# Optimization experiments

Measured on AMD Instinct MI355X. Metric: run time of the kernel, lower is better.

Reference implementation:

```python
import jax, jax.numpy as jnp
import numpy as np

N_NODES = 50000
N_EDGES = 800000
N_GRAPHS = 64
IN_DIM = 128
HID4 = 256  # hidden_dim * 4
OUT_DIM = 256
EPS = 1e-5


def setup_inputs() -> dict:
    key = jax.random.key(0)
    ks = jax.random.split(key, 11)
    x = jax.random.normal(ks[0], (N_NODES, IN_DIM), jnp.float32)
    w = jax.random.uniform(ks[1], (N_EDGES,), jnp.float32)
    src = jax.random.randint(ks[2], (N_EDGES,), 0, N_NODES, dtype=jnp.int32)
    dst = jax.random.randint(ks[3], (N_EDGES,), 0, N_NODES, dtype=jnp.int32)
    graph_ids = jnp.sort(jax.random.randint(ks[4], (N_NODES,), 0, N_GRAPHS, dtype=jnp.int32))
    W1 = jax.random.normal(ks[5], (IN_DIM, HID4), jnp.float32) * 0.05
    Wfc = jax.random.normal(ks[6], (IN_DIM, HID4), jnp.float32) * 0.05
    gamma = jnp.ones((HID4,), jnp.float32)
    beta = jnp.zeros((HID4,), jnp.float32)
    W2 = jax.random.normal(ks[7], (2 * HID4, HID4), jnp.float32) * 0.05
    W3 = jax.random.normal(ks[8], (HID4, OUT_DIM), jnp.float32) * 0.05
    return {"x": x, "w": w, "W1": W1, "Wfc": Wfc, "gamma": gamma, "beta": beta,
            "W2": W2, "W3": W3, "src": src, "dst": dst, "graph_ids": graph_ids}


def _agg(h, src, dst, w, n):
    # edge-weighted SpMM: sum_{e: dst(e)=v} w_e * h[src(e)]
    return jax.ops.segment_sum(h[src] * w[:, None], dst, num_segments=n)


def _graph_conv(h, W, src, dst, w, out_norm, in_norm, n):
    # DGL GraphConv, norm='both', no bias, with edge_weight.
    h = h * out_norm  # D_out^{-1/2} on source side
    din, dout = W.shape
    if din > dout:  # DGL applies W first when it shrinks the width
        h = _agg(h @ W, src, dst, w, n)
    else:
        h = _agg(h, src, dst, w, n) @ W
    return h * in_norm  # D_in^{-1/2} on destination side


def _layer_norm(h, gamma, beta):
    mu = jnp.mean(h, axis=-1, keepdims=True)
    var = jnp.var(h, axis=-1, keepdims=True)
    return (h - mu) * jax.lax.rsqrt(var + EPS) * gamma + beta


def reference(x, w, W1, Wfc, gamma, beta, W2, W3, src, dst, graph_ids):
    n = x.shape[0]
    ones_e = jnp.ones(src.shape[0], jnp.float32)
    out_deg = jnp.maximum(jax.ops.segment_sum(ones_e, src, num_segments=n), 1.0)
    in_deg = jnp.maximum(jax.ops.segment_sum(ones_e, dst, num_segments=n), 1.0)
    out_norm = (out_deg ** -0.5)[:, None]
    in_norm = (in_deg ** -0.5)[:, None]

    x1 = jax.nn.relu(_graph_conv(x, W1, src, dst, w, out_norm, in_norm, n))
    f1 = jax.nn.relu(_layer_norm(x @ Wfc, gamma, beta))
    x1f1 = jnp.concatenate((x1, f1), axis=1)  # [N, 512]
    x2 = jax.nn.relu(_graph_conv(x1f1, W2, src, dst, w, out_norm, in_norm, n))
    x3 = jax.nn.relu(_graph_conv(x2, W3, src, dst, w, out_norm, in_norm, n))
    # dgl.sum_nodes: per-graph segment-sum readout
    readout = jax.ops.segment_sum(x3, graph_ids, num_segments=N_GRAPHS)
    return readout
```

## Files before the change

### kernel.cpp

```cpp
#include <hip/hip_runtime.h>

#define NN 50000
#define NE 800000
#define NG 64
#define EPSF 1e-5f

typedef __bf16 bf16x8 __attribute__((ext_vector_type(8)));
typedef float f32x4 __attribute__((ext_vector_type(4)));

#define AS1 __attribute__((address_space(1)))
#define AS3 __attribute__((address_space(3)))

__device__ __forceinline__ void gl_lds16(const unsigned short* g, unsigned short* l) {
#if __has_builtin(__builtin_amdgcn_global_load_lds)
  __builtin_amdgcn_global_load_lds((const AS1 void*)g, (AS3 void*)l, 16, 0, 0);
#else
  *(uint4*)l = *(const uint4*)g;
#endif
}

__device__ __forceinline__ unsigned short f2bf(float f) {
  unsigned u = __builtin_bit_cast(unsigned, f);
  u += 0x7fff + ((u >> 16) & 1);
  return (unsigned short)(u >> 16);
}
__device__ __forceinline__ float bf_lo(unsigned u) {
  return __builtin_bit_cast(float, u << 16);
}
__device__ __forceinline__ float bf_hi(unsigned u) {
  return __builtin_bit_cast(float, u & 0xffff0000u);
}

#define NB_H 64
#define EC   12500
#define HWORDS 12500
#define XB   1563
#define XTOT 1600000
#define WTB  256
__global__ __launch_bounds__(1024) void prep_kernel(
    const int* __restrict__ src, const int* __restrict__ dst,
    unsigned char* __restrict__ hout, unsigned char* __restrict__ hin,
    int* __restrict__ rank,
    const float* __restrict__ x, unsigned short* __restrict__ xb,
    const float* __restrict__ W1, const float* __restrict__ Wfc,
    const float* __restrict__ W2, const float* __restrict__ W3,
    unsigned short* __restrict__ W1t, unsigned short* __restrict__ Wfct,
    unsigned short* __restrict__ W2t, unsigned short* __restrict__ W3t) {
  __shared__ unsigned hist[HWORDS];
  int b = blockIdx.x;
  int tid = threadIdx.x;
  if (b < NB_H) {
    int e0 = b * EC;
#pragma unroll
    for (int ph = 0; ph < 2; ph++) {
      const int* key = ph ? src : dst;
      unsigned char* gh = (ph ? hout : hin) + (size_t)b * NN;
      for (int i = tid; i < HWORDS; i += 1024) hist[i] = 0u;
      __syncthreads();
      for (int i = tid; i < EC; i += 1024) {
        int k = key[e0 + i];
        int sh = (k & 3) << 3;
        unsigned old = atomicAdd(&hist[k >> 2], 1u << sh);
        if (ph == 0) rank[e0 + i] = (int)((old >> sh) & 0xffu);
      }
      __syncthreads();
      unsigned* gw = (unsigned*)gh;
      for (int i = tid; i < HWORDS; i += 1024) gw[i] = hist[i];
      __syncthreads();
    }
  } else if (b < NB_H + XB) {
    int i = (b - NB_H) * 1024 + tid;
    if (i < XTOT) {
      float4 v = ((const float4*)x)[i];
      uint2 pk;
      pk.x = (unsigned)f2bf(v.x) | ((unsigned)f2bf(v.y) << 16);
      pk.y = (unsigned)f2bf(v.z) | ((unsigned)f2bf(v.w) << 16);
      ((uint2*)xb)[i] = pk;
    }
  } else {
    int i = (b - NB_H - XB) * 1024 + tid;
    const float* W; unsigned short* Wt; int K, local;
    if (i < 32768)       { W = W1;  Wt = W1t;  K = 128; local = i; }
    else if (i < 65536)  { W = Wfc; Wt = Wfct; K = 128; local = i - 32768; }
    else if (i < 196608) { W = W2;  Wt = W2t;  K = 512; local = i - 65536; }
    else                 { W = W3;  Wt = W3t;  K = 256; local = i - 196608; }
    int n = local / K, k = local - n * K;
    Wt[local] = f2bf(W[(size_t)k * 256 + n]);
  }
}

__global__ void norms_scan1(const unsigned char* __restrict__ hout,
                            unsigned char* __restrict__ hin,
                            int* __restrict__ din,
                            float* __restrict__ onorm, float* __restrict__ inorm,
                            int* __restrict__ bsum, int n) {
  int i = blockIdx.x * 256 + threadIdx.x;
  int d = 0;
  if (i < n) {
    int a = 0;
    for (int b = 0; b < NB_H; b++) a += hout[(size_t)b * NN + i];
    int run = 0;
    for (int b = 0; b < NB_H; b++) {
      int t = hin[(size_t)b * NN + i];
      hin[(size_t)b * NN + i] = (unsigned char)run;
      run += t;
    }
    d = run;
    din[i] = run;
    onorm[i] = rsqrtf((float)(a > 1 ? a : 1));
    inorm[i] = rsqrtf((float)(d > 1 ? d : 1));
  }
  int v = d;
#pragma unroll
  for (int off = 32; off > 0; off >>= 1) v += __shfl_down(v, off);
  __shared__ int ws[4];
  int wave = threadIdx.x >> 6, lane = threadIdx.x & 63;
  if (lane == 0) ws[wave] = v;
  __syncthreads();
  if (threadIdx.x == 0) bsum[blockIdx.x] = ws[0] + ws[1] + ws[2] + ws[3];
}

__global__ void scan3_kernel(const int* __restrict__ din, const int* __restrict__ bsum,
                             int* __restrict__ rp, int n, int nb) {
  int t = threadIdx.x;
  int lane = t & 63, wave = t >> 6;
  int bj = (t < nb) ? bsum[t] : 0;
  int pre = (t < (int)blockIdx.x) ? bj : 0;
  int p = pre, q = bj;
#pragma unroll
  for (int off = 32; off > 0; off >>= 1) {
    p += __shfl_down(p, off);
    q += __shfl_down(q, off);
  }
  __shared__ int red[8];
  __shared__ int baseS, totS;
  if (lane == 0) { red[wave] = p; red[4 + wave] = q; }
  __syncthreads();
  if (t == 0) {
    baseS = red[0] + red[1] + red[2] + red[3];
    totS  = red[4] + red[5] + red[6] + red[7];
  }
  __syncthreads();
  int i = blockIdx.x * 256 + t;
  int v = (i < n) ? din[i] : 0;
  __shared__ int tmp[256];
  tmp[t] = v;
  __syncthreads();
  for (int off = 1; off < 256; off <<= 1) {
    int x = (t >= off) ? tmp[t - off] : 0;
    __syncthreads();
    tmp[t] += x;
    __syncthreads();
  }
  if (i < n) rp[i] = tmp[t] - v + baseS;
  if (blockIdx.x == gridDim.x - 1 && t == 0) rp[n] = totS;
}

__global__ void fill_kernel(const int* __restrict__ src, const int* __restrict__ dst,
                            const float* __restrict__ w, const float* __restrict__ onorm,
                            const float* __restrict__ inorm,
                            const int* __restrict__ rp, const int* __restrict__ rank,
                            const unsigned char* __restrict__ binBase,
                            uint2* __restrict__ edge, int E) {
  int e = blockIdx.x * 256 + threadIdx.x;
  if (e < E) {
    int d = dst[e], s = src[e];
    int b = e / EC;
    int pos = rp[d] + (int)binBase[(size_t)b * NN + d] + rank[e];
    float wv = w[e] * onorm[s] * inorm[d];
    edge[pos] = make_uint2((unsigned)s, __builtin_bit_cast(unsigned, wv));
  }
}

template <int RELU, int NU>
__global__ __launch_bounds__(64) void spmm_bf16(
    const unsigned short* __restrict__ feat, int ldf,
    const int* __restrict__ rp, const uint2* __restrict__ edge,
    unsigned short* __restrict__ out, int ldo) {
  int v = blockIdx.x;
  int t = threadIdx.x;
  int beg = rp[v], end = rp[v + 1];
  float acc[2 * NU];
#pragma unroll
  for (int i = 0; i < 2 * NU; i++) acc[i] = 0.f;
  const unsigned short* base = feat + t * (2 * NU);
  int e = beg;
  for (; e + 8 <= end; e += 8) {
    int s[8]; float ww[8];
#pragma unroll
    for (int k = 0; k < 8; k++) {
      uint2 q = edge[e + k];
      s[k] = (int)q.x;
      ww[k] = __builtin_bit_cast(float, q.y);
    }
    unsigned u[8][NU];
#pragma unroll
    for (int k = 0; k < 8; k++) {
      const unsigned* pr = (const unsigned*)&base[(size_t)s[k] * ldf];
      if (NU == 2) { uint2 q = *(const uint2*)pr; u[k][0] = q.x; u[k][NU - 1] = q.y; }
      else u[k][0] = pr[0];
    }
#pragma unroll
    for (int k = 0; k < 8; k++)
#pragma unroll
      for (int j = 0; j < NU; j++) {
        acc[2 * j]     += ww[k] * bf_lo(u[k][j]);
        acc[2 * j + 1] += ww[k] * bf_hi(u[k][j]);
      }
  }
  for (; e < end; e++) {
    uint2 qe = edge[e];
    float w0 = __builtin_bit_cast(float, qe.y);
    const unsigned* pr = (const unsigned*)&base[(size_t)qe.x * ldf];
    unsigned u[NU];
    if (NU == 2) { uint2 q = *(const uint2*)pr; u[0] = q.x; u[NU - 1] = q.y; }
    else u[0] = pr[0];
#pragma unroll
    for (int j = 0; j < NU; j++) {
      acc[2 * j]     += w0 * bf_lo(u[j]);
      acc[2 * j + 1] += w0 * bf_hi(u[j]);
    }
  }
  unsigned o[NU];
#pragma unroll
  for (int j = 0; j < NU; j++) {
    float a = acc[2 * j], b = acc[2 * j + 1];
    if (RELU) { a = fmaxf(a, 0.f); b = fmaxf(b, 0.f); }
    o[j] = (unsigned)f2bf(a) | ((unsigned)f2bf(b) << 16);
  }
  unsigned* po = (unsigned*)&out[(size_t)v * ldo + t * (2 * NU)];
  if (NU == 2) *(uint2*)po = make_uint2(o[0], o[NU - 1]);
  else po[0] = o[0];
}

__device__ __forceinline__ void gemm256_body(
    const unsigned short* __restrict__ A, int lda,
    const unsigned short* __restrict__ Bt, int K,
    unsigned short* __restrict__ C, int ldc, int col_off, int M,
    int relu, unsigned short* As, unsigned short* Bs) {
  const int tid = threadIdx.x;
  const int lane = tid & 63;
  const int w = tid >> 6;
  const int q = lane >> 4;
  const int r16 = lane & 15;
  const int m0 = blockIdx.x * 128;

  f32x4 acc[8][4];
#pragma unroll
  for (int i = 0; i < 8; i++)
#pragma unroll
    for (int j = 0; j < 4; j++) acc[i][j] = (f32x4){0.f, 0.f, 0.f, 0.f};

  int ga0 = m0 + (2 * w) * 16 + r16;     if (ga0 >= M) ga0 = M - 1;
  int ga1 = m0 + (2 * w + 1) * 16 + r16; if (ga1 >= M) ga1 = M - 1;
  const unsigned short* pa0 = A + (size_t)ga0 * lda + q * 8;
  const unsigned short* pa1 = A + (size_t)ga1 * lda + q * 8;
  const unsigned short* pbt[4];
#pragma unroll
  for (int t = 0; t < 4; t++) {
    int gn = (4 * w + t) * 16 + r16;
    pbt[t] = Bt + (size_t)gn * K + q * 8;
  }

  for (int k0 = 0; k0 < K; k0 += 32) {
    __syncthreads();
    gl_lds16(pa0 + k0, &As[(2 * w) * 512 + lane * 8]);
    gl_lds16(pa1 + k0, &As[(2 * w + 1) * 512 + lane * 8]);
#pragma unroll
    for (int t = 0; t < 4; t++)
      gl_lds16(pbt[t] + k0, &Bs[(4 * w + t) * 512 + lane * 8]);
    __syncthreads();

    bf16x8 bfr[4];
#pragma unroll
    for (int j = 0; j < 4; j++)
      bfr[j] = *(const bf16x8*)&Bs[(4 * w + j) * 512 + lane * 8];
#pragma unroll
    for (int i = 0; i < 8; i++) {
      bf16x8 af = *(const bf16x8*)&As[i * 512 + lane * 8];
#pragma unroll
      for (int j = 0; j < 4; j++)
        acc[i][j] = __builtin_amdgcn_mfma_f32_16x16x32_bf16(af, bfr[j], acc[i][j], 0, 0, 0);
    }
  }

#pragma unroll
  for (int i = 0; i < 8; i++) {
    int rbase = m0 + i * 16 + q * 4;
#pragma unroll
    for (int r = 0; r < 4; r++) {
      int gm = rbase + r;
      if (gm >= M) continue;
#pragma unroll
      for (int j = 0; j < 4; j++) {
        float v = acc[i][j][r];
        if (relu) v = fmaxf(v, 0.f);
        int gn = col_off + (4 * w + j) * 16 + r16;
        C[(size_t)gm * ldc + gn] = f2bf(v);
      }
    }
  }
}

__global__ __launch_bounds__(256) void gemm12_kernel(
    const unsigned short* __restrict__ A0, const unsigned short* __restrict__ B0,
    const unsigned short* __restrict__ A1, const unsigned short* __restrict__ B1,
    unsigned short* __restrict__ C, int M) {
  __shared__ unsigned short As[8 * 512];
  __shared__ unsigned short Bs[16 * 512];
  int z = blockIdx.z;
  gemm256_body(z ? A1 : A0, 128, z ? B1 : B0, 128, C, 512, z * 256, M, z == 0, As, Bs);
}

__global__ __launch_bounds__(256) void gemm_kernel(
    const unsigned short* __restrict__ A, int lda,
    const unsigned short* __restrict__ Bt, int K,
    unsigned short* __restrict__ C, int ldc, int M, int relu) {
  __shared__ unsigned short As[8 * 512];
  __shared__ unsigned short Bs[16 * 512];
  gemm256_body(A, lda, Bt, K, C, ldc, 0, M, relu, As, Bs);
}

__global__ void ln_relu_bf16(unsigned short* __restrict__ h, int ld,
                             const float* __restrict__ gamma,
                             const float* __restrict__ beta) {
  int v = blockIdx.x;
  int f = threadIdx.x;
  float val = bf_lo((unsigned)h[(size_t)v * ld + f]);
  float s = val, qq = val * val;
#pragma unroll
  for (int off = 32; off > 0; off >>= 1) {
    s += __shfl_down(s, off);
    qq += __shfl_down(qq, off);
  }
  __shared__ float ws_[5], wq_[5];
  int wave = f >> 6, lane = f & 63;
  if (lane == 0) { ws_[wave] = s; wq_[wave] = qq; }
  __syncthreads();
  if (f == 0) {
    float S = 0, Q = 0;
    for (int i = 0; i < 4; i++) { S += ws_[i]; Q += wq_[i]; }
    ws_[4] = S; wq_[4] = Q;
  }
  __syncthreads();
  float mean = ws_[4] * (1.f / 256.f);
  float var = wq_[4] * (1.f / 256.f) - mean * mean;
  float y = (val - mean) * rsqrtf(var + EPSF) * gamma[f] + beta[f];
  h[(size_t)v * ld + f] = f2bf(y > 0.f ? y : 0.f);
}

__global__ void readout_kernel(const unsigned short* __restrict__ x3,
                               const int* __restrict__ gid,
                               float* __restrict__ out, int n) {
  int g = blockIdx.x;
  int part = blockIdx.y;
  int f = threadIdx.x;
  int lo = 0, hi = n;
  while (lo < hi) { int mid = (lo + hi) >> 1; if (gid[mid] < g) lo = mid + 1; else hi = mid; }
  int s = lo;
  lo = s; hi = n;
  while (lo < hi) { int mid = (lo + hi) >> 1; if (gid[mid] < g + 1) lo = mid + 1; else hi = mid; }
  int e = lo;
  int len = e - s;
  if (len <= 0) return;
  int chunk = (len + 7) / 8;
  int cs = s + part * chunk;
  int ce = cs + chunk; if (ce > e) ce = e;
  if (cs >= ce) return;
  float acc = 0.f;
  for (int v = cs; v < ce; v++) acc += bf_lo((unsigned)x3[(size_t)v * 256 + f]);
  atomicAdd(&out[g * 256 + f], acc);
}


extern "C" void kernel_launch(void* const* d_in, const int* in_sizes, int n_in,
                              void* d_out, int out_size, void* d_ws, size_t ws_size,
                              hipStream_t stream) {
  const float* x     = (const float*)d_in[0];
  const float* w     = (const float*)d_in[1];
  const float* W1    = (const float*)d_in[2];
  const float* Wfc   = (const float*)d_in[3];
  const float* gamma = (const float*)d_in[4];
  const float* beta  = (const float*)d_in[5];
  const float* W2    = (const float*)d_in[6];
  const float* W3    = (const float*)d_in[7];
  const int*   src   = (const int*)d_in[8];
  const int*   dst   = (const int*)d_in[9];
  const int*   gid   = (const int*)d_in[10];
  float* out = (float*)d_out;

  const int N = NN, E = NE;

  char* p = (char*)d_ws;
  auto alloc = [&](size_t bytes) {
    char* r = p;
    p += (bytes + 255) & ~(size_t)255;
    return r;
  };
  unsigned char* hout = (unsigned char*)alloc((size_t)NB_H * N);
  unsigned char* hin  = (unsigned char*)alloc((size_t)NB_H * N);
  int*   din     = (int*)alloc((size_t)N * 4);
  float* onorm   = (float*)alloc((size_t)N * 4);
  float* inorm   = (float*)alloc((size_t)N * 4);
  int*   row_ptr = (int*)alloc((size_t)(N + 1) * 4);
  int*   bsum    = (int*)alloc(256 * 4);
  int*   rank    = (int*)alloc((size_t)E * 4);
  uint2* edge    = (uint2*)alloc((size_t)E * 8);
  unsigned short* xb    = (unsigned short*)alloc((size_t)N * 128 * 2);
  unsigned short* aggX  = (unsigned short*)alloc((size_t)N * 128 * 2);
  unsigned short* x1f1  = (unsigned short*)alloc((size_t)N * 512 * 2);
  unsigned short* y2    = (unsigned short*)alloc((size_t)N * 256 * 2);
  unsigned short* x2    = (unsigned short*)alloc((size_t)N * 256 * 2);
  unsigned short* aggx2 = (unsigned short*)alloc((size_t)N * 256 * 2);
  unsigned short* W1t   = (unsigned short*)alloc((size_t)256 * 128 * 2);
  unsigned short* Wfct  = (unsigned short*)alloc((size_t)256 * 128 * 2);
  unsigned short* W2t   = (unsigned short*)alloc((size_t)256 * 512 * 2);
  unsigned short* W3t   = (unsigned short*)alloc((size_t)256 * 256 * 2);
  unsigned short* x3 = x1f1;

  hipMemsetAsync(out, 0, (size_t)NG * 256 * 4, stream);

  const int nbS = (N + 255) / 256;

  prep_kernel<<<NB_H + XB + WTB, 1024, 0, stream>>>(src, dst, hout, hin, rank,
                                                    x, xb, W1, Wfc, W2, W3,
                                                    W1t, Wfct, W2t, W3t);
  norms_scan1<<<nbS, 256, 0, stream>>>(hout, hin, din, onorm, inorm, bsum, N);
  scan3_kernel<<<nbS, 256, 0, stream>>>(din, bsum, row_ptr, N, nbS);
  fill_kernel<<<(E + 255) / 256, 256, 0, stream>>>(src, dst, w, onorm, inorm, row_ptr,
                                                   rank, hin, edge, E);

  dim3 ggrid((N + 127) / 128, 1);
  dim3 ggridz((N + 127) / 128, 1, 2);

  spmm_bf16<0, 1><<<N, 64, 0, stream>>>(xb, 128, row_ptr, edge, aggX, 128);
  gemm12_kernel<<<ggridz, 256, 0, stream>>>(aggX, W1t, xb, Wfct, x1f1, N);
  ln_relu_bf16<<<N, 256, 0, stream>>>(x1f1 + 256, 512, gamma, beta);
  gemm_kernel<<<ggrid, 256, 0, stream>>>(x1f1, 512, W2t, 512, y2, 256, N, 0);
  spmm_bf16<1, 2><<<N, 64, 0, stream>>>(y2, 256, row_ptr, edge, x2, 256);
  spmm_bf16<0, 2><<<N, 64, 0, stream>>>(x2, 256, row_ptr, edge, aggx2, 256);
  gemm_kernel<<<ggrid, 256, 0, stream>>>(aggx2, 256, W3t, 256, x3, 256, N, 1);
  readout_kernel<<<dim3(NG, 8), 256, 0, stream>>>(x3, gid, out, N);
}
```

Measured before the change: 461.4 us.

## Double-buffer GEMM LDS tiles and split N across a 2D 128x128 block grid

Rewrites the bf16 MFMA GEMM body to use 128x128 output tiles with a 2x2 wave layout and a K-step of 64, double-buffering A and B tiles in LDS so the next tile's global-to-LDS loads overlap the current MFMA work. The grid gains a second dimension over N (two column tiles per 256-wide output), which doubles the block count and halves per-thread accumulators. The cost is double the LDS per block (64 KB), which may limit occupancy, and A tiles are now loaded twice, once per column tile.

```diff
diff --git a/kernel.cpp b/kernel.cpp
--- a/kernel.cpp
+++ b/kernel.cpp
@@ -233,60 +233,83 @@
   else po[0] = o[0];
 }
 
-__device__ __forceinline__ void gemm256_body(
+__device__ __forceinline__ void gemm_db_body(
     const unsigned short* __restrict__ A, int lda,
     const unsigned short* __restrict__ Bt, int K,
     unsigned short* __restrict__ C, int ldc, int col_off, int M,
-    int relu, unsigned short* As, unsigned short* Bs) {
+    int relu, unsigned short (*As)[8192], unsigned short (*Bs)[8192]) {
   const int tid = threadIdx.x;
   const int lane = tid & 63;
   const int w = tid >> 6;
+  const int wm = w >> 1, wn = w & 1;
+  const int m0 = blockIdx.x * 128;
+  const int n0 = blockIdx.y * 128;
   const int q = lane >> 4;
   const int r16 = lane & 15;
-  const int m0 = blockIdx.x * 128;
-
-  f32x4 acc[8][4];
-#pragma unroll
-  for (int i = 0; i < 8; i++)
+
+  f32x4 acc[4][4];
+#pragma unroll
+  for (int i = 0; i < 4; i++)
 #pragma unroll
     for (int j = 0; j < 4; j++) acc[i][j] = (f32x4){0.f, 0.f, 0.f, 0.f};
 
-  int ga0 = m0 + (2 * w) * 16 + r16;     if (ga0 >= M) ga0 = M - 1;
-  int ga1 = m0 + (2 * w + 1) * 16 + r16; if (ga1 >= M) ga1 = M - 1;
-  const unsigned short* pa0 = A + (size_t)ga0 * lda + q * 8;
-  const unsigned short* pa1 = A + (size_t)ga1 * lda + q * 8;
-  const unsigned short* pbt[4];
-#pragma unroll
-  for (int t = 0; t < 4; t++) {
-    int gn = (4 * w + t) * 16 + r16;
-    pbt[t] = Bt + (size_t)gn * K + q * 8;
-  }
-
-  for (int k0 = 0; k0 < K; k0 += 32) {
+  const unsigned short* pa[4];
+  const unsigned short* pb[4];
+#pragma unroll
+  for (int i = 0; i < 4; i++) {
+    int ch = i * 256 + tid;
+    int sub = ch >> 6, sl = ch & 63;
+    int mi = sub >> 1, kk = sub & 1;
+    int row = mi * 16 + (sl & 15);
+    int kc = kk * 32 + (sl >> 4) * 8;
+    int gm = m0 + row; if (gm >= M) gm = M - 1;
+    pa[i] = A + (size_t)gm * lda + kc;
+    int gn = n0 + row;
+    pb[i] = Bt + (size_t)gn * K + kc;
+  }
+
+  const int NT = K >> 6;
+#pragma unroll
+  for (int i = 0; i < 4; i++) {
+    int ch8 = (i * 256 + tid) * 8;
+    gl_lds16(pa[i], &As[0][ch8]);
+    gl_lds16(pb[i], &Bs[0][ch8]);
+  }
+  __syncthreads();
+
+  int cur = 0;
+  for (int t = 0; t < NT; t++) {
+    if (t + 1 < NT) {
+      int nk = (t + 1) << 6;
+#pragma unroll
+      for (int i = 0; i < 4; i++) {
+        int ch8 = (i * 256 + tid) * 8;
+        gl_lds16(pa[i] + nk, &As[cur ^ 1][ch8]);
+        gl_lds16(pb[i] + nk, &Bs[cur ^ 1][ch8]);
+      }
+    }
+#pragma unroll
+    for (int kk = 0; kk < 2; kk++) {
+      bf16x8 af[4], bfr[4];
+#pragma unroll
+      for (int i = 0; i < 4; i++)
+        af[i] = *(const bf16x8*)&As[cur][((wm * 4 + i) * 2 + kk) * 512 + lane * 8];
+#pragma unroll
+      for (int j = 0; j < 4; j++)
+        bfr[j] = *(const bf16x8*)&Bs[cur][((wn * 4 + j) * 2 + kk) * 512 + lane * 8];
+#pragma unroll
+      for (int i = 0; i < 4; i++)
+#pragma unroll
+        for (int j = 0; j < 4; j++)
+          acc[i][j] = __builtin_amdgcn_mfma_f32_16x16x32_bf16(af[i], bfr[j], acc[i][j], 0, 0, 0);
+    }
     __syncthreads();
-    gl_lds16(pa0 + k0, &As[(2 * w) * 512 + lane * 8]);
-    gl_lds16(pa1 + k0, &As[(2 * w + 1) * 512 + lane * 8]);
-#pragma unroll
-    for (int t = 0; t < 4; t++)
-      gl_lds16(pbt[t] + k0, &Bs[(4 * w + t) * 512 + lane * 8]);
-    __syncthreads();
-
-    bf16x8 bfr[4];
-#pragma unroll
-    for (int j = 0; j < 4; j++)
-      bfr[j] = *(const bf16x8*)&Bs[(4 * w + j) * 512 + lane * 8];
-#pragma unroll
-    for (int i = 0; i < 8; i++) {
-      bf16x8 af = *(const bf16x8*)&As[i * 512 + lane * 8];
-#pragma unroll
-      for (int j = 0; j < 4; j++)
-        acc[i][j] = __builtin_amdgcn_mfma_f32_16x16x32_bf16(af, bfr[j], acc[i][j], 0, 0, 0);
-    }
-  }
-
-#pragma unroll
-  for (int i = 0; i < 8; i++) {
-    int rbase = m0 + i * 16 + q * 4;
+    cur ^= 1;
+  }
+
+#pragma unroll
+  for (int i = 0; i < 4; i++) {
+    int rbase = m0 + wm * 64 + i * 16 + q * 4;
 #pragma unroll
     for (int r = 0; r < 4; r++) {
       int gm = rbase + r;
@@ -295,7 +318,7 @@
       for (int j = 0; j < 4; j++) {
         float v = acc[i][j][r];
         if (relu) v = fmaxf(v, 0.f);
-        int gn = col_off + (4 * w + j) * 16 + r16;
+        int gn = col_off + n0 + wn * 64 + j * 16 + r16;
         C[(size_t)gm * ldc + gn] = f2bf(v);
       }
     }
@@ -306,19 +329,19 @@
     const unsigned short* __restrict__ A0, const unsigned short* __restrict__ B0,
     const unsigned short* __restrict__ A1, const unsigned short* __restrict__ B1,
     unsigned short* __restrict__ C, int M) {
-  __shared__ unsigned short As[8 * 512];
-  __shared__ unsigned short Bs[16 * 512];
+  __shared__ unsigned short As[2][8192];
+  __shared__ unsigned short Bs[2][8192];
   int z = blockIdx.z;
-  gemm256_body(z ? A1 : A0, 128, z ? B1 : B0, 128, C, 512, z * 256, M, z == 0, As, Bs);
+  gemm_db_body(z ? A1 : A0, 128, z ? B1 : B0, 128, C, 512, z * 256, M, z == 0, As, Bs);
 }
 
 __global__ __launch_bounds__(256) void gemm_kernel(
     const unsigned short* __restrict__ A, int lda,
     const unsigned short* __restrict__ Bt, int K,
     unsigned short* __restrict__ C, int ldc, int M, int relu) {
-  __shared__ unsigned short As[8 * 512];
-  __shared__ unsigned short Bs[16 * 512];
-  gemm256_body(A, lda, Bt, K, C, ldc, 0, M, relu, As, Bs);
+  __shared__ unsigned short As[2][8192];
+  __shared__ unsigned short Bs[2][8192];
+  gemm_db_body(A, lda, Bt, K, C, ldc, 0, M, relu, As, Bs);
 }
 
 __global__ void ln_relu_bf16(unsigned short* __restrict__ h, int ld,
@@ -430,8 +453,8 @@
   fill_kernel<<<(E + 255) / 256, 256, 0, stream>>>(src, dst, w, onorm, inorm, row_ptr,
                                                    rank, hin, edge, E);
 
-  dim3 ggrid((N + 127) / 128, 1);
-  dim3 ggridz((N + 127) / 128, 1, 2);
+  dim3 ggrid((N + 127) / 128, 2);
+  dim3 ggridz((N + 127) / 128, 2, 2);
 
   spmm_bf16<0, 1><<<N, 64, 0, stream>>>(xb, 128, row_ptr, edge, aggX, 128);
   gemm12_kernel<<<ggridz, 256, 0, stream>>>(aggX, W1t, xb, Wfct, x1f1, N);
```

Result: faster. 432.8 us (-6.2%).
